# Optimization experiments

Hardware: AMD Instinct MI355X
Metric: run time of the kernel (lower is better)

## Reference

```python
import jax, jax.numpy as jnp
import numpy as np

EPS = 1e-5

def layernorm(x, g, b):
    mu = jnp.mean(x, axis=-1, keepdims=True)
    var = jnp.var(x, axis=-1, keepdims=True)
    return (x - mu) * jax.lax.rsqrt(var + EPS) * g + b

DIM = 1024; CTX = 1024; HEADS = 12; DHEAD = 64; INNER = HEADS * DHEAD
B = 4; F = 2048; J = 1024

def setup_inputs() -> dict:
    key = jax.random.key(0)
    ks = jax.random.split(key, 8)
    s = lambda d: 1.0 / np.sqrt(d)
    return {
        "x": jax.random.normal(ks[0], (B, F, DIM), jnp.float32),
        "tab_x": jax.random.normal(ks[1], (B, J, CTX), jnp.float32),
        "tab_g": jnp.ones((CTX,), jnp.float32), "tab_b": jnp.zeros((CTX,), jnp.float32),
        "vid_g": jnp.ones((DIM,), jnp.float32), "vid_b": jnp.zeros((DIM,), jnp.float32),
        "Wq": jax.random.normal(ks[2], (DIM, INNER), jnp.float32) * s(DIM),
        "Wk": jax.random.normal(ks[3], (CTX, INNER), jnp.float32) * s(CTX),
        "Wv": jax.random.normal(ks[4], (CTX, INNER), jnp.float32) * s(CTX),
        "q_g": jnp.ones((INNER,), jnp.float32), "q_b": jnp.zeros((INNER,), jnp.float32),
        "k_g": jnp.ones((INNER,), jnp.float32), "k_b": jnp.zeros((INNER,), jnp.float32),
        "Wo": jax.random.normal(ks[5], (INNER, DIM), jnp.float32) * s(INNER),
        "bo": jnp.zeros((DIM,), jnp.float32),
    }

def reference(x, tab_x, tab_g, tab_b, vid_g, vid_b, Wq, Wk, Wv, q_g, q_b, k_g, k_b, Wo, bo):
    scale = DHEAD ** -0.5
    kv_in = layernorm(tab_x, tab_g, tab_b)                      # [b,j,ctx]
    q = layernorm(layernorm(x, vid_g, vid_b) @ Wq, q_g, q_b)    # [b,f,inner]
    k = layernorm(kv_in @ Wk, k_g, k_b)                         # [b,j,inner]
    v = kv_in @ Wv                                              # [b,j,inner]
    split = lambda t: t.reshape(t.shape[0], t.shape[1], HEADS, DHEAD).transpose(0, 2, 1, 3)
    q, k, v = split(q) * scale, split(k), split(v)              # [b,h,*,d]
    sim = jnp.einsum('bhid,bhjd->bhij', q, k)
    attn = jax.nn.softmax(sim, axis=-1)
    out = jnp.einsum('bhij,bhjd->bhid', attn, v)                # [b,h,f,d]
    out = out.transpose(0, 2, 1, 3).reshape(x.shape[0], x.shape[1], INNER)
    return out @ Wo + bo
```

## Files before the change

kernel.cpp:

```cpp
#include <hip/hip_runtime.h>

typedef unsigned short u16;
typedef float  f32x4   __attribute__((ext_vector_type(4)));
typedef float  f32x16  __attribute__((ext_vector_type(16)));
typedef __bf16 bf16x8  __attribute__((ext_vector_type(8)));
typedef u16    u16x4   __attribute__((ext_vector_type(4)));

#define DEV __device__ __forceinline__

DEV u16 f2bf(float f) {
  union { float f; unsigned u; } x; x.f = f;
  unsigned r = x.u + 0x7fffu + ((x.u >> 16) & 1u);
  return (u16)(r >> 16);
}
DEV float bf2f(u16 b) { union { unsigned u; float f; } c; c.u = (unsigned)b << 16; return c.f; }

DEV unsigned cvtpk(float lo, float hi) {
  unsigned r;
  asm("v_cvt_pk_bf16_f32 %0, %1, %2" : "=v"(r) : "v"(lo), "v"(hi));
  return r;
}
#if __has_builtin(__builtin_amdgcn_exp2f)
DEV float fexp2(float x) { return __builtin_amdgcn_exp2f(x); }
#else
DEV float fexp2(float x) { return __builtin_exp2f(x); }
#endif

DEV f32x4 mfma16(bf16x8 a, bf16x8 b, f32x4 c) {
  return __builtin_amdgcn_mfma_f32_16x16x32_bf16(a, b, c, 0, 0, 0);
}
DEV f32x16 mfma32(bf16x8 a, bf16x8 b, f32x16 c) {
  return __builtin_amdgcn_mfma_f32_32x32x16_bf16(a, b, c, 0, 0, 0);
}

DEV void gload16(const void* g, void* l) {
  __builtin_amdgcn_global_load_lds(
      (__attribute__((address_space(1))) void*)g,
      (__attribute__((address_space(3))) void*)l, 16, 0, 0);
}

#define WAIT(N) asm volatile("s_waitcnt vmcnt(" #N ")" ::: "memory")
#define BAR()   __builtin_amdgcn_s_barrier()

template<typename LOADER>
DEV void ln_body(LOADER load, const float* __restrict__ g, const float* __restrict__ bta,
                 u16* __restrict__ yrow, int C, float outscale, float* red)
{
  const int tid = threadIdx.x;
  const int n4 = C >> 2;
  f32x4 v = {0.f, 0.f, 0.f, 0.f};
  if (tid < n4) v = load(tid);
  float s1 = v[0] + v[1] + v[2] + v[3];
  float s2 = v[0]*v[0] + v[1]*v[1] + v[2]*v[2] + v[3]*v[3];
#pragma unroll
  for (int o = 32; o > 0; o >>= 1) {
    s1 += __shfl_xor(s1, o, 64);
    s2 += __shfl_xor(s2, o, 64);
  }
  const int lane = tid & 63, wv = tid >> 6;
  if (lane == 0) { red[wv] = s1; red[4 + wv] = s2; }
  __syncthreads();
  s1 = red[0] + red[1] + red[2] + red[3];
  s2 = red[4] + red[5] + red[6] + red[7];
  const float mu = s1 / C;
  const float rs = rsqrtf(s2 / C - mu * mu + 1e-5f);
  if (tid < n4) {
    f32x4 gg = *(const f32x4*)(g + 4 * tid);
    f32x4 bb = *(const f32x4*)(bta + 4 * tid);
    u16x4 o4;
#pragma unroll
    for (int j = 0; j < 4; ++j)
      o4[j] = f2bf(((v[j] - mu) * rs * gg[j] + bb[j]) * outscale);
    *(u16x4*)(yrow + 4 * tid) = o4;
  }
}

__global__ __launch_bounds__(256)
void prep(const float* __restrict__ Wq, const float* __restrict__ Wk,
          const float* __restrict__ Wv, const float* __restrict__ Wo,
          u16* __restrict__ WqT, u16* __restrict__ WkvT, u16* __restrict__ WoT,
          const float* __restrict__ tabx, const float* __restrict__ tab_g,
          const float* __restrict__ tab_b,
          const float* __restrict__ x, const float* __restrict__ vid_g,
          const float* __restrict__ vid_b,
          u16* __restrict__ kvn, u16* __restrict__ xn)
{
  __shared__ float t[32][33];
  __shared__ float red[8];
  const int bid = blockIdx.x;
  const int tid = threadIdx.x;
  if (bid < 3840) {
    const float* src; u16* dst; int K, N, k0, n0;
    if (bid < 3072) {
      const int w = bid / 768, r = bid % 768;
      src = (w == 0) ? Wq : (w == 1) ? Wk : Wv;
      dst = (w == 0) ? WqT : (w == 1) ? WkvT : WkvT + (size_t)768 * 1024;
      K = 1024; N = 768; k0 = (r % 32) * 32; n0 = (r / 32) * 32;
    } else {
      const int r = bid - 3072;
      src = Wo; dst = WoT;
      K = 768; N = 1024; k0 = (r % 24) * 32; n0 = (r / 24) * 32;
    }
    const int tx = tid & 31, ty = tid >> 5;
#pragma unroll
    for (int i = ty; i < 32; i += 8)
      t[i][tx] = src[(size_t)(k0 + i) * N + n0 + tx];
    __syncthreads();
#pragma unroll
    for (int i = ty; i < 32; i += 8)
      dst[(size_t)(n0 + i) * K + k0 + tx] = f2bf(t[tx][i]);
  } else {
    const int r = bid - 3840;
    const float* xr; const float *g, *bb; u16* y;
    if (r < 4096) { xr = tabx + (size_t)r * 1024; g = tab_g; bb = tab_b;
                    y = kvn + (size_t)r * 1024; }
    else { const int rr = r - 4096; xr = x + (size_t)rr * 1024; g = vid_g;
           bb = vid_b; y = xn + (size_t)rr * 1024; }
    ln_body([&](int i) { return *(const f32x4*)(xr + 4 * i); }, g, bb, y, 1024, 1.0f, red);
  }
}

__global__ __launch_bounds__(256)
void gemm_qkv(const u16* __restrict__ xn, const u16* __restrict__ kvn,
              const u16* __restrict__ WqT, const u16* __restrict__ WkvT,
              u16* __restrict__ q_pre, u16* __restrict__ k_pre, u16* __restrict__ vT)
{
  __shared__ __align__(16) u16 As[2][128 * 32];
  __shared__ __align__(16) u16 Bs[2][128 * 32];
  const int bid = blockIdx.x;
  const int tid  = threadIdx.x;
  const int lane = tid & 63;
  const int wave = tid >> 6;
  const bool isq = bid >= 384;
  const u16* A; const u16* Bt; int bm, bn;
  if (!isq) { A = kvn;  Bt = WkvT; bm = (bid & 31) * 128;  bn = (bid >> 5) * 128; }
  else { const int r = bid - 384; A = xn; Bt = WqT; bm = (r & 63) * 128; bn = (r >> 6) * 128; }
  const int wm = (wave >> 1) * 64;
  const int wn = (wave & 1) * 64;
  const int fr = lane & 15;
  const int fkb = (lane >> 4) * 16;

  f32x4 acc[4][4] = {};

  const char* pA0; const char* pA1; const char* pB0; const char* pB1;
  {
    const char* gA0 = (const char*)(A  + (size_t)bm * 1024);
    const char* gB0 = (const char*)(Bt + (size_t)bn * 1024);
    const int o0 = tid * 16, o1 = tid * 16 + 4096;
    const int r0 = o0 >> 6, r1 = o1 >> 6;
    const int s0 = (o0 & 63) ^ (((r0 >> 1) & 3) << 4);
    const int s1 = (o1 & 63) ^ (((r1 >> 1) & 3) << 4);
    pA0 = gA0 + (size_t)r0 * 2048 + s0;  pA1 = gA0 + (size_t)r1 * 2048 + s1;
    pB0 = gB0 + (size_t)r0 * 2048 + s0;  pB1 = gB0 + (size_t)r1 * 2048 + s1;
  }
  char* const dA0 = (char*)&As[0][0] + wave * 1024;
  char* const dB0 = (char*)&Bs[0][0] + wave * 1024;

  auto stage = [&](int buf) {
    char* da = dA0 + (buf << 13);
    char* db = dB0 + (buf << 13);
    gload16(pA0, da);        gload16(pB0, db);
    gload16(pA1, da + 4096); gload16(pB1, db + 4096);
    pA0 += 64; pA1 += 64; pB0 += 64; pB1 += 64;
  };

  int offA[4], offB[4];
#pragma unroll
  for (int m = 0; m < 4; ++m) {
    const int row = wm + m * 16 + fr;
    offA[m] = row * 64 + (fkb ^ (((row >> 1) & 3) << 4));
  }
#pragma unroll
  for (int n = 0; n < 4; ++n) {
    const int row = wn + n * 16 + fr;
    offB[n] = row * 64 + (fkb ^ (((row >> 1) & 3) << 4));
  }

  auto step = [&](int cur) {
    const char* ba = (const char*)&As[0][0] + (cur << 13);
    const char* bb = (const char*)&Bs[0][0] + (cur << 13);
    bf16x8 af[4], bg[4];
#pragma unroll
    for (int m = 0; m < 4; ++m) af[m] = *(const bf16x8*)(ba + offA[m]);
#pragma unroll
    for (int n = 0; n < 4; ++n) bg[n] = *(const bf16x8*)(bb + offB[n]);
#pragma unroll
    for (int m = 0; m < 4; ++m)
#pragma unroll
      for (int n = 0; n < 4; ++n)
        acc[m][n] = mfma16(af[m], bg[n], acc[m][n]);
  };

  stage(0);
#pragma unroll 1
  for (int t = 0; t < 31; ++t) {
    stage((t & 1) ^ 1);
    WAIT(4);
    BAR();
    step(t & 1);
    BAR();
    asm volatile("" ::: "memory");
  }
  WAIT(0);
  BAR();
  step(31 & 1);

  const int orow0 = bm + wm + 4 * (lane >> 4);
  const int ocol0 = bn + wn + fr;
#pragma unroll
  for (int m = 0; m < 4; ++m)
#pragma unroll
    for (int n = 0; n < 4; ++n) {
      const int row0 = orow0 + m * 16;
      const int col  = ocol0 + n * 16;
      if (isq) {
#pragma unroll
        for (int r = 0; r < 4; ++r)
          q_pre[(size_t)(row0 + r) * 768 + col] = f2bf(acc[m][n][r]);
      } else if (col < 768) {
#pragma unroll
        for (int r = 0; r < 4; ++r)
          k_pre[(size_t)(row0 + r) * 768 + col] = f2bf(acc[m][n][r]);
      } else {
        const int c2 = col - 768, hh = c2 >> 6, dd = c2 & 63;
        const int bb2 = row0 >> 10, jj = row0 & 1023;
        u16x4 o4;
#pragma unroll
        for (int r = 0; r < 4; ++r) o4[r] = f2bf(acc[m][n][r]);
        *(u16x4*)(vT + ((size_t)(bb2 * 12 + hh) * 64 + dd) * 1024 + jj) = o4;
      }
    }
}

__global__ __launch_bounds__(256)
void ln_qk(const u16* __restrict__ k_pre, const float* __restrict__ k_g,
           const float* __restrict__ k_b, u16* __restrict__ kb,
           const u16* __restrict__ q_pre, const float* __restrict__ q_g,
           const float* __restrict__ q_b, u16* __restrict__ qb)
{
  __shared__ float red[8];
  const int bid = blockIdx.x;
  const bool isk = bid < 4096;
  const int row = isk ? bid : bid - 4096;
  const u16* xr = (isk ? k_pre : q_pre) + (size_t)row * 768;
  u16* y = (isk ? kb : qb) + (size_t)row * 768;
  const float sc = isk ? 1.0f : 0.125f * 1.44269504089f;
  ln_body([&](int i) {
    const u16x4 raw = *(const u16x4*)(xr + 4 * i);
    f32x4 v;
#pragma unroll
    for (int j = 0; j < 4; ++j) v[j] = bf2f(raw[j]);
    return v;
  }, isk ? k_g : q_g, isk ? k_b : q_b, y, 768, sc, red);
}

__global__ __launch_bounds__(256, 3)
void attn7(const u16* __restrict__ q, const u16* __restrict__ k,
           const u16* __restrict__ vT, u16* __restrict__ att)
{
  __shared__ __align__(16) u16 Ks[2][64 * 64];
  __shared__ __align__(16) u16 Vs[2][64 * 64];
  __shared__ __align__(16) u16 osm[4][32][72];

  const int bh = blockIdx.x;
  const int b = bh / 12, h = bh - b * 12;
  const int tid = threadIdx.x, lane = tid & 63, wave = tid >> 6;
  const int lq  = lane & 31;
  const int hi5 = lane >> 5;
  const int qrow = blockIdx.y * 128 + wave * 32 + lq;

  const u16* qp = q + (size_t)(b * 2048 + qrow) * 768 + h * 64 + hi5 * 8;
  bf16x8 qf[4];
#pragma unroll
  for (int ds = 0; ds < 4; ++ds) qf[ds] = *(const bf16x8*)(qp + ds * 16);

  f32x16 ot0 = {}, ot1 = {};
  float l0 = 0.f, l1 = 0.f, l2 = 0.f, l3 = 0.f;

  const int rsw0 = (lq & 7) << 4;

  const char* pk0; const char* pk1; const char* pv0; const char* pv1;
  {
    const char* kg = (const char*)k + (size_t)(b * 1024) * 1536 + h * 128;
    const char* vg = (const char*)vT + (size_t)bh * 64 * 2048;
    const int o0 = tid * 16, o1 = tid * 16 + 4096;
    const int r0 = o0 >> 7, r1 = o1 >> 7;
    const int s0 = (o0 & 127) ^ ((r0 & 7) << 4);
    const int s1 = (o1 & 127) ^ ((r1 & 7) << 4);
    pk0 = kg + (size_t)r0 * 1536 + s0;  pk1 = kg + (size_t)r1 * 1536 + s1;
    pv0 = vg + (size_t)r0 * 2048 + s0;  pv1 = vg + (size_t)r1 * 2048 + s1;
  }
  char* const dK0 = (char*)&Ks[0][0] + wave * 1024;
  char* const dV0 = (char*)&Vs[0][0] + wave * 1024;

  auto stage = [&](int buf) {
    char* dk = dK0 + (buf << 13);
    char* dv = dV0 + (buf << 13);
    gload16(pk0, dk);        gload16(pv0, dv);
    gload16(pk1, dk + 4096); gload16(pv1, dv + 4096);
    pk0 += 64 * 1536; pk1 += 64 * 1536;
    pv0 += 128;       pv1 += 128;
  };

  auto step = [&](int cur) {
    f32x16 st0 = {}, st1 = {};
    __builtin_amdgcn_s_setprio(1);
#pragma unroll
    for (int ds = 0; ds < 4; ++ds) {
      const int cb = ds * 32 + hi5 * 16;
      const bf16x8 k0 = *(const bf16x8*)((const char*)&Ks[cur][0] + lq * 128 + (cb ^ rsw0));
      const bf16x8 k1 = *(const bf16x8*)((const char*)&Ks[cur][0] + (lq + 32) * 128 + (cb ^ rsw0));
      st0 = mfma32(k0, qf[ds], st0);
      st1 = mfma32(k1, qf[ds], st1);
    }
    __builtin_amdgcn_s_setprio(0);
#pragma unroll
    for (int r = 0; r < 16; r += 4) {
      float p0 = fexp2(st0[r]);     st0[r]     = p0; l0 += p0;
      float p1 = fexp2(st0[r + 1]); st0[r + 1] = p1; l1 += p1;
      float p2 = fexp2(st0[r + 2]); st0[r + 2] = p2; l2 += p2;
      float p3 = fexp2(st0[r + 3]); st0[r + 3] = p3; l3 += p3;
    }
#pragma unroll
    for (int r = 0; r < 16; r += 4) {
      float p0 = fexp2(st1[r]);     st1[r]     = p0; l0 += p0;
      float p1 = fexp2(st1[r + 1]); st1[r + 1] = p1; l1 += p1;
      float p2 = fexp2(st1[r + 2]); st1[r + 2] = p2; l2 += p2;
      float p3 = fexp2(st1[r + 3]); st1[r + 3] = p3; l3 += p3;
    }
    __builtin_amdgcn_s_setprio(1);
#pragma unroll
    for (int s4 = 0; s4 < 4; ++s4) {
      const int u = (s4 & 1) * 8;
      float a0, a1, a2, a3, b0, b1, b2, b3;
      if (s4 < 2) {
        a0 = st0[u]; a1 = st0[u + 1]; a2 = st0[u + 2]; a3 = st0[u + 3];
        b0 = st0[u + 4]; b1 = st0[u + 5]; b2 = st0[u + 6]; b3 = st0[u + 7];
      } else {
        a0 = st1[u]; a1 = st1[u + 1]; a2 = st1[u + 2]; a3 = st1[u + 3];
        b0 = st1[u + 4]; b1 = st1[u + 5]; b2 = st1[u + 6]; b3 = st1[u + 7];
      }
      const unsigned L0 = cvtpk(a0, a1), L1 = cvtpk(a2, a3);
      const unsigned H0 = cvtpk(b0, b1), H1 = cvtpk(b2, b3);
      const auto w02 = __builtin_amdgcn_permlane32_swap(L0, H0, false, false);
      const auto w13 = __builtin_amdgcn_permlane32_swap(L1, H1, false, false);
      union BU { unsigned w[4]; bf16x8 v; } pu;
      pu.w[0] = w02[0]; pu.w[1] = w13[0]; pu.w[2] = w02[1]; pu.w[3] = w13[1];
      const int cb = s4 * 32 + hi5 * 16;
      const bf16x8 v0 = *(const bf16x8*)((const char*)&Vs[cur][0] + lq * 128 + (cb ^ rsw0));
      const bf16x8 v1 = *(const bf16x8*)((const char*)&Vs[cur][0] + (lq + 32) * 128 + (cb ^ rsw0));
      ot0 = mfma32(v0, pu.v, ot0);
      ot1 = mfma32(v1, pu.v, ot1);
    }
    __builtin_amdgcn_s_setprio(0);
  };

  stage(0);
#pragma unroll 1
  for (int tt = 0; tt < 7; ++tt) {
    stage(1);
    WAIT(4);
    BAR();
    step(0);
    BAR();
    stage(0);
    WAIT(4);
    BAR();
    step(1);
    BAR();
    asm volatile("" ::: "memory");
  }
  stage(1);
  WAIT(4);
  BAR();
  step(0);
  BAR();
  WAIT(0);
  BAR();
  step(1);

  float l = (l0 + l1) + (l2 + l3);
  l += __shfl_xor(l, 32, 64);
  const float inv = 1.0f / l;
#pragma unroll
  for (int r = 0; r < 16; ++r) {
    const int d0 = (r & 3) + 8 * (r >> 2) + 4 * hi5;
    osm[wave][lq][d0]      = f2bf(ot0[r] * inv);
    osm[wave][lq][32 + d0] = f2bf(ot1[r] * inv);
  }
  asm volatile("s_waitcnt lgkmcnt(0)" ::: "memory");
  const int col = (lane & 7) * 8;
#pragma unroll
  for (int pass = 0; pass < 4; ++pass) {
    const int row = pass * 8 + (lane >> 3);
    const bf16x8 vv = *(const bf16x8*)&osm[wave][row][col];
    const int qg = blockIdx.y * 128 + wave * 32 + row;
    *(bf16x8*)(att + (size_t)(b * 2048 + qg) * 768 + h * 64 + col) = vv;
  }
}

__global__ __launch_bounds__(256)
void gemm_o(const u16* __restrict__ A, const u16* __restrict__ Bt,
            float* __restrict__ Cp, const float* __restrict__ bias)
{
  __shared__ __align__(16) u16 As[2][128 * 32];
  __shared__ __align__(16) u16 Bs[2][128 * 32];
  const int tid  = threadIdx.x;
  const int lane = tid & 63;
  const int wave = tid >> 6;
  const int bm = blockIdx.x * 128;
  const int bn = blockIdx.y * 128;
  const int wm = (wave >> 1) * 64;
  const int wn = (wave & 1) * 64;
  const int fr = lane & 15;
  const int fkb = (lane >> 4) * 16;

  f32x4 acc[4][4] = {};

  const char* pA0; const char* pA1; const char* pB0; const char* pB1;
  {
    const char* gA0 = (const char*)(A  + (size_t)bm * 768);
    const char* gB0 = (const char*)(Bt + (size_t)bn * 768);
    const int o0 = tid * 16, o1 = tid * 16 + 4096;
    const int r0 = o0 >> 6, r1 = o1 >> 6;
    const int s0 = (o0 & 63) ^ (((r0 >> 1) & 3) << 4);
    const int s1 = (o1 & 63) ^ (((r1 >> 1) & 3) << 4);
    pA0 = gA0 + (size_t)r0 * 1536 + s0;  pA1 = gA0 + (size_t)r1 * 1536 + s1;
    pB0 = gB0 + (size_t)r0 * 1536 + s0;  pB1 = gB0 + (size_t)r1 * 1536 + s1;
  }
  char* const dA0 = (char*)&As[0][0] + wave * 1024;
  char* const dB0 = (char*)&Bs[0][0] + wave * 1024;

  auto stage = [&](int buf) {
    char* da = dA0 + (buf << 13);
    char* db = dB0 + (buf << 13);
    gload16(pA0, da);        gload16(pB0, db);
    gload16(pA1, da + 4096); gload16(pB1, db + 4096);
    pA0 += 64; pA1 += 64; pB0 += 64; pB1 += 64;
  };

  int offA[4], offB[4];
#pragma unroll
  for (int m = 0; m < 4; ++m) {
    const int row = wm + m * 16 + fr;
    offA[m] = row * 64 + (fkb ^ (((row >> 1) & 3) << 4));
  }
#pragma unroll
  for (int n = 0; n < 4; ++n) {
    const int row = wn + n * 16 + fr;
    offB[n] = row * 64 + (fkb ^ (((row >> 1) & 3) << 4));
  }

  auto step = [&](int cur) {
    const char* ba = (const char*)&As[0][0] + (cur << 13);
    const char* bb = (const char*)&Bs[0][0] + (cur << 13);
    bf16x8 af[4], bg[4];
#pragma unroll
    for (int m = 0; m < 4; ++m) af[m] = *(const bf16x8*)(ba + offA[m]);
#pragma unroll
    for (int n = 0; n < 4; ++n) bg[n] = *(const bf16x8*)(bb + offB[n]);
#pragma unroll
    for (int m = 0; m < 4; ++m)
#pragma unroll
      for (int n = 0; n < 4; ++n)
        acc[m][n] = mfma16(af[m], bg[n], acc[m][n]);
  };

  stage(0);
#pragma unroll 1
  for (int t = 0; t < 23; ++t) {
    stage((t & 1) ^ 1);
    WAIT(4);
    BAR();
    step(t & 1);
    BAR();
    asm volatile("" ::: "memory");
  }
  WAIT(0);
  BAR();
  step(23 & 1);

  const int orow0 = bm + wm + 4 * (lane >> 4);
  const int ocol0 = bn + wn + fr;
#pragma unroll
  for (int m = 0; m < 4; ++m)
#pragma unroll
    for (int n = 0; n < 4; ++n)
#pragma unroll
      for (int r = 0; r < 4; ++r) {
        const int row = orow0 + m * 16 + r;
        const int col = ocol0 + n * 16;
        Cp[(size_t)row * 1024 + col] = acc[m][n][r] + bias[col];
      }
}

extern "C" void kernel_launch(void* const* d_in, const int* in_sizes, int n_in,
                              void* d_out, int out_size, void* d_ws, size_t ws_size,
                              hipStream_t stream)
{
  const float* x     = (const float*)d_in[0];
  const float* tabx  = (const float*)d_in[1];
  const float* tab_g = (const float*)d_in[2];
  const float* tab_b = (const float*)d_in[3];
  const float* vid_g = (const float*)d_in[4];
  const float* vid_b = (const float*)d_in[5];
  const float* Wq    = (const float*)d_in[6];
  const float* Wk    = (const float*)d_in[7];
  const float* Wv    = (const float*)d_in[8];
  const float* q_g   = (const float*)d_in[9];
  const float* q_b   = (const float*)d_in[10];
  const float* k_g   = (const float*)d_in[11];
  const float* k_b   = (const float*)d_in[12];
  const float* Wo    = (const float*)d_in[13];
  const float* bo    = (const float*)d_in[14];

  char* ws = (char*)d_ws;
  const size_t O_WQT  = 0;
  const size_t O_WKVT = O_WQT  + (size_t)768 * 1024 * 2;
  const size_t O_WOT  = O_WKVT + (size_t)1536 * 1024 * 2;
  const size_t O_XN   = O_WOT  + (size_t)1024 * 768 * 2;
  const size_t O_KVN  = O_XN   + (size_t)8192 * 1024 * 2;
  const size_t O_QPRE = O_KVN  + (size_t)4096 * 1024 * 2;
  const size_t O_KPRE = O_QPRE + (size_t)8192 * 768 * 2;
  const size_t O_QB   = O_KPRE + (size_t)4096 * 768 * 2;
  const size_t O_KB   = O_QB   + (size_t)8192 * 768 * 2;
  const size_t O_VT   = O_KB   + (size_t)4096 * 768 * 2;
  const size_t O_ATT  = O_QPRE;

  u16*   WqT   = (u16*)(ws + O_WQT);
  u16*   WkvT  = (u16*)(ws + O_WKVT);
  u16*   WoT   = (u16*)(ws + O_WOT);
  u16*   xn    = (u16*)(ws + O_XN);
  u16*   kvn   = (u16*)(ws + O_KVN);
  u16*   q_pre = (u16*)(ws + O_QPRE);
  u16*   k_pre = (u16*)(ws + O_KPRE);
  u16*   qb    = (u16*)(ws + O_QB);
  u16*   kb    = (u16*)(ws + O_KB);
  u16*   vT    = (u16*)(ws + O_VT);
  u16*   attb  = (u16*)(ws + O_ATT);

  prep<<<16128, 256, 0, stream>>>(Wq, Wk, Wv, Wo, WqT, WkvT, WoT,
                                  tabx, tab_g, tab_b, x, vid_g, vid_b, kvn, xn);
  gemm_qkv<<<768, 256, 0, stream>>>(xn, kvn, WqT, WkvT, q_pre, k_pre, vT);
  ln_qk<<<12288, 256, 0, stream>>>(k_pre, k_g, k_b, kb, q_pre, q_g, q_b, qb);
  attn7<<<dim3(48, 16), 256, 0, stream>>>(qb, kb, vT, attb);
  gemm_o<<<dim3(64, 8), 256, 0, stream>>>(attb, WoT, (float*)d_out, bo);
}
```

Baseline: 128.8 us.

## Process two 32-row query tiles per wave in attention to reuse K/V fragments

Each wave in the attention kernel now handles 64 query rows instead of 32, as two independent accumulator sets that share every K and V fragment read from LDS. Each block covers 256 query rows, so the grid halves and each block loads K/V tiles from global memory half as often in total. The cost is roughly double the accumulator and score registers, which is why launch bounds drop from 3 to 2 blocks per CU. Fewer blocks (384) and lower occupancy may hurt latency hiding.

```diff
diff --git a/kernel.cpp b/kernel.cpp
--- a/kernel.cpp
+++ b/kernel.cpp
@@ -254,8 +254,8 @@
   }, isk ? k_g : q_g, isk ? k_b : q_b, y, 768, sc, red);
 }
 
-__global__ __launch_bounds__(256, 3)
-void attn7(const u16* __restrict__ q, const u16* __restrict__ k,
+__global__ __launch_bounds__(256, 2)
+void attn8(const u16* __restrict__ q, const u16* __restrict__ k,
            const u16* __restrict__ vT, u16* __restrict__ att)
 {
   __shared__ __align__(16) u16 Ks[2][64 * 64];
@@ -267,15 +267,20 @@
   const int tid = threadIdx.x, lane = tid & 63, wave = tid >> 6;
   const int lq  = lane & 31;
   const int hi5 = lane >> 5;
-  const int qrow = blockIdx.y * 128 + wave * 32 + lq;
-
-  const u16* qp = q + (size_t)(b * 2048 + qrow) * 768 + h * 64 + hi5 * 8;
-  bf16x8 qf[4];
-#pragma unroll
-  for (int ds = 0; ds < 4; ++ds) qf[ds] = *(const bf16x8*)(qp + ds * 16);
-
-  f32x16 ot0 = {}, ot1 = {};
-  float l0 = 0.f, l1 = 0.f, l2 = 0.f, l3 = 0.f;
+  const int qrow0 = blockIdx.y * 256 + wave * 64;
+
+  const u16* qpA = q + (size_t)(b * 2048 + qrow0 + lq) * 768 + h * 64 + hi5 * 8;
+  const u16* qpB = qpA + (size_t)32 * 768;
+  bf16x8 qfa[4], qfb[4];
+#pragma unroll
+  for (int ds = 0; ds < 4; ++ds) {
+    qfa[ds] = *(const bf16x8*)(qpA + ds * 16);
+    qfb[ds] = *(const bf16x8*)(qpB + ds * 16);
+  }
+
+  f32x16 oa0 = {}, oa1 = {}, ob0 = {}, ob1 = {};
+  float la0 = 0.f, la1 = 0.f, la2 = 0.f, la3 = 0.f;
+  float lb0 = 0.f, lb1 = 0.f, lb2 = 0.f, lb3 = 0.f;
 
   const int rsw0 = (lq & 7) << 4;
 
@@ -303,54 +308,81 @@
   };
 
   auto step = [&](int cur) {
-    f32x16 st0 = {}, st1 = {};
+    f32x16 sa0 = {}, sa1 = {}, sb0 = {}, sb1 = {};
     __builtin_amdgcn_s_setprio(1);
 #pragma unroll
     for (int ds = 0; ds < 4; ++ds) {
       const int cb = ds * 32 + hi5 * 16;
       const bf16x8 k0 = *(const bf16x8*)((const char*)&Ks[cur][0] + lq * 128 + (cb ^ rsw0));
       const bf16x8 k1 = *(const bf16x8*)((const char*)&Ks[cur][0] + (lq + 32) * 128 + (cb ^ rsw0));
-      st0 = mfma32(k0, qf[ds], st0);
-      st1 = mfma32(k1, qf[ds], st1);
+      sa0 = mfma32(k0, qfa[ds], sa0);
+      sa1 = mfma32(k1, qfa[ds], sa1);
+      sb0 = mfma32(k0, qfb[ds], sb0);
+      sb1 = mfma32(k1, qfb[ds], sb1);
     }
     __builtin_amdgcn_s_setprio(0);
 #pragma unroll
     for (int r = 0; r < 16; r += 4) {
-      float p0 = fexp2(st0[r]);     st0[r]     = p0; l0 += p0;
-      float p1 = fexp2(st0[r + 1]); st0[r + 1] = p1; l1 += p1;
-      float p2 = fexp2(st0[r + 2]); st0[r + 2] = p2; l2 += p2;
-      float p3 = fexp2(st0[r + 3]); st0[r + 3] = p3; l3 += p3;
+      float p0 = fexp2(sa0[r]);     sa0[r]     = p0; la0 += p0;
+      float p1 = fexp2(sa0[r + 1]); sa0[r + 1] = p1; la1 += p1;
+      float p2 = fexp2(sa0[r + 2]); sa0[r + 2] = p2; la2 += p2;
+      float p3 = fexp2(sa0[r + 3]); sa0[r + 3] = p3; la3 += p3;
     }
 #pragma unroll
     for (int r = 0; r < 16; r += 4) {
-      float p0 = fexp2(st1[r]);     st1[r]     = p0; l0 += p0;
-      float p1 = fexp2(st1[r + 1]); st1[r + 1] = p1; l1 += p1;
-      float p2 = fexp2(st1[r + 2]); st1[r + 2] = p2; l2 += p2;
-      float p3 = fexp2(st1[r + 3]); st1[r + 3] = p3; l3 += p3;
+      float p0 = fexp2(sa1[r]);     sa1[r]     = p0; la0 += p0;
+      float p1 = fexp2(sa1[r + 1]); sa1[r + 1] = p1; la1 += p1;
+      float p2 = fexp2(sa1[r + 2]); sa1[r + 2] = p2; la2 += p2;
+      float p3 = fexp2(sa1[r + 3]); sa1[r + 3] = p3; la3 += p3;
+    }
+#pragma unroll
+    for (int r = 0; r < 16; r += 4) {
+      float p0 = fexp2(sb0[r]);     sb0[r]     = p0; lb0 += p0;
+      float p1 = fexp2(sb0[r + 1]); sb0[r + 1] = p1; lb1 += p1;
+      float p2 = fexp2(sb0[r + 2]); sb0[r + 2] = p2; lb2 += p2;
+      float p3 = fexp2(sb0[r + 3]); sb0[r + 3] = p3; lb3 += p3;
+    }
+#pragma unroll
+    for (int r = 0; r < 16; r += 4) {
+      float p0 = fexp2(sb1[r]);     sb1[r]     = p0; lb0 += p0;
+      float p1 = fexp2(sb1[r + 1]); sb1[r + 1] = p1; lb1 += p1;
+      float p2 = fexp2(sb1[r + 2]); sb1[r + 2] = p2; lb2 += p2;
+      float p3 = fexp2(sb1[r + 3]); sb1[r + 3] = p3; lb3 += p3;
     }
     __builtin_amdgcn_s_setprio(1);
 #pragma unroll
     for (int s4 = 0; s4 < 4; ++s4) {
       const int u = (s4 & 1) * 8;
-      float a0, a1, a2, a3, b0, b1, b2, b3;
+      float a0,a1,a2,a3,b0,b1,b2,b3, c0,c1,c2,c3,d0_,d1_,d2_,d3_;
       if (s4 < 2) {
-        a0 = st0[u]; a1 = st0[u + 1]; a2 = st0[u + 2]; a3 = st0[u + 3];
-        b0 = st0[u + 4]; b1 = st0[u + 5]; b2 = st0[u + 6]; b3 = st0[u + 7];
+        a0=sa0[u];a1=sa0[u+1];a2=sa0[u+2];a3=sa0[u+3];
+        b0=sa0[u+4];b1=sa0[u+5];b2=sa0[u+6];b3=sa0[u+7];
+        c0=sb0[u];c1=sb0[u+1];c2=sb0[u+2];c3=sb0[u+3];
+        d0_=sb0[u+4];d1_=sb0[u+5];d2_=sb0[u+6];d3_=sb0[u+7];
       } else {
-        a0 = st1[u]; a1 = st1[u + 1]; a2 = st1[u + 2]; a3 = st1[u + 3];
-        b0 = st1[u + 4]; b1 = st1[u + 5]; b2 = st1[u + 6]; b3 = st1[u + 7];
+        a0=sa1[u];a1=sa1[u+1];a2=sa1[u+2];a3=sa1[u+3];
+        b0=sa1[u+4];b1=sa1[u+5];b2=sa1[u+6];b3=sa1[u+7];
+        c0=sb1[u];c1=sb1[u+1];c2=sb1[u+2];c3=sb1[u+3];
+        d0_=sb1[u+4];d1_=sb1[u+5];d2_=sb1[u+6];d3_=sb1[u+7];
       }
-      const unsigned L0 = cvtpk(a0, a1), L1 = cvtpk(a2, a3);
-      const unsigned H0 = cvtpk(b0, b1), H1 = cvtpk(b2, b3);
-      const auto w02 = __builtin_amdgcn_permlane32_swap(L0, H0, false, false);
-      const auto w13 = __builtin_amdgcn_permlane32_swap(L1, H1, false, false);
-      union BU { unsigned w[4]; bf16x8 v; } pu;
-      pu.w[0] = w02[0]; pu.w[1] = w13[0]; pu.w[2] = w02[1]; pu.w[3] = w13[1];
+      const unsigned La0 = cvtpk(a0, a1), La1 = cvtpk(a2, a3);
+      const unsigned Ha0 = cvtpk(b0, b1), Ha1 = cvtpk(b2, b3);
+      const auto wa02 = __builtin_amdgcn_permlane32_swap(La0, Ha0, false, false);
+      const auto wa13 = __builtin_amdgcn_permlane32_swap(La1, Ha1, false, false);
+      union BU { unsigned w[4]; bf16x8 v; } pa, pb;
+      pa.w[0] = wa02[0]; pa.w[1] = wa13[0]; pa.w[2] = wa02[1]; pa.w[3] = wa13[1];
+      const unsigned Lb0 = cvtpk(c0, c1), Lb1 = cvtpk(c2, c3);
+      const unsigned Hb0 = cvtpk(d0_, d1_), Hb1 = cvtpk(d2_, d3_);
+      const auto wb02 = __builtin_amdgcn_permlane32_swap(Lb0, Hb0, false, false);
+      const auto wb13 = __builtin_amdgcn_permlane32_swap(Lb1, Hb1, false, false);
+      pb.w[0] = wb02[0]; pb.w[1] = wb13[0]; pb.w[2] = wb02[1]; pb.w[3] = wb13[1];
       const int cb = s4 * 32 + hi5 * 16;
       const bf16x8 v0 = *(const bf16x8*)((const char*)&Vs[cur][0] + lq * 128 + (cb ^ rsw0));
       const bf16x8 v1 = *(const bf16x8*)((const char*)&Vs[cur][0] + (lq + 32) * 128 + (cb ^ rsw0));
-      ot0 = mfma32(v0, pu.v, ot0);
-      ot1 = mfma32(v1, pu.v, ot1);
+      oa0 = mfma32(v0, pa.v, oa0);
+      oa1 = mfma32(v1, pa.v, oa1);
+      ob0 = mfma32(v0, pb.v, ob0);
+      ob1 = mfma32(v1, pb.v, ob1);
     }
     __builtin_amdgcn_s_setprio(0);
   };
@@ -379,22 +411,40 @@
   BAR();
   step(1);
 
-  float l = (l0 + l1) + (l2 + l3);
-  l += __shfl_xor(l, 32, 64);
-  const float inv = 1.0f / l;
+  float lA = (la0 + la1) + (la2 + la3);
+  lA += __shfl_xor(lA, 32, 64);
+  float lB = (lb0 + lb1) + (lb2 + lb3);
+  lB += __shfl_xor(lB, 32, 64);
+  const float invA = 1.0f / lA, invB = 1.0f / lB;
+
+  const int col = (lane & 7) * 8;
 #pragma unroll
   for (int r = 0; r < 16; ++r) {
     const int d0 = (r & 3) + 8 * (r >> 2) + 4 * hi5;
-    osm[wave][lq][d0]      = f2bf(ot0[r] * inv);
-    osm[wave][lq][32 + d0] = f2bf(ot1[r] * inv);
+    osm[wave][lq][d0]      = f2bf(oa0[r] * invA);
+    osm[wave][lq][32 + d0] = f2bf(oa1[r] * invA);
   }
   asm volatile("s_waitcnt lgkmcnt(0)" ::: "memory");
-  const int col = (lane & 7) * 8;
 #pragma unroll
   for (int pass = 0; pass < 4; ++pass) {
     const int row = pass * 8 + (lane >> 3);
     const bf16x8 vv = *(const bf16x8*)&osm[wave][row][col];
-    const int qg = blockIdx.y * 128 + wave * 32 + row;
+    const int qg = qrow0 + row;
+    *(bf16x8*)(att + (size_t)(b * 2048 + qg) * 768 + h * 64 + col) = vv;
+  }
+  asm volatile("s_waitcnt lgkmcnt(0)" ::: "memory");
+#pragma unroll
+  for (int r = 0; r < 16; ++r) {
+    const int d0 = (r & 3) + 8 * (r >> 2) + 4 * hi5;
+    osm[wave][lq][d0]      = f2bf(ob0[r] * invB);
+    osm[wave][lq][32 + d0] = f2bf(ob1[r] * invB);
+  }
+  asm volatile("s_waitcnt lgkmcnt(0)" ::: "memory");
+#pragma unroll
+  for (int pass = 0; pass < 4; ++pass) {
+    const int row = pass * 8 + (lane >> 3);
+    const bf16x8 vv = *(const bf16x8*)&osm[wave][row][col];
+    const int qg = qrow0 + 32 + row;
     *(bf16x8*)(att + (size_t)(b * 2048 + qg) * 768 + h * 64 + col) = vv;
   }
 }
@@ -543,6 +593,6 @@
                                   tabx, tab_g, tab_b, x, vid_g, vid_b, kvn, xn);
   gemm_qkv<<<768, 256, 0, stream>>>(xn, kvn, WqT, WkvT, q_pre, k_pre, vT);
   ln_qk<<<12288, 256, 0, stream>>>(k_pre, k_g, k_b, kb, q_pre, q_g, q_b, qb);
-  attn7<<<dim3(48, 16), 256, 0, stream>>>(qb, kb, vT, attb);
+  attn8<<<dim3(48, 8), 256, 0, stream>>>(qb, kb, vT, attb);
   gemm_o<<<dim3(64, 8), 256, 0, stream>>>(attb, WoT, (float*)d_out, bo);
 }
```

Result: slower. 131.4 us (+2.0%).
